# Kernel optimization log

Measured on AMD Instinct MI355X. Metric: run time of the kernel, lower is better.

Reference implementation:

```python
import jax, jax.numpy as jnp
import numpy as np

# dims: T tokens, E experts, D model dim, F ffn dim, C per-expert capacity, K top-k routing
T, E, D, F, C, K = 4096, 8, 1024, 4096, 1536, 2


def setup_inputs() -> dict:
    key = jax.random.key(0)
    k_x, k_lg, k_w1, k_w2 = jax.random.split(key, 4)
    x = jax.random.normal(k_x, (T, D), jnp.float32)
    # external router: top-K of logits per token, softmax weights over kept logits
    logits = jax.random.normal(k_lg, (T, E), jnp.float32)
    topv, topi = jax.lax.top_k(logits, K)                      # (T,K)
    rows = jnp.arange(T)[:, None]
    route_mask = jnp.zeros((T, E), bool).at[rows, topi].set(True)
    route_weight = jnp.zeros((T, E), jnp.float32).at[rows, topi].set(
        jax.nn.softmax(topv, axis=-1))
    # stacked homogeneous expert MLP params (E leading axis, as in _stack_group)
    W1 = jax.random.normal(k_w1, (E, D, F), jnp.float32) / np.sqrt(D)
    b1 = jnp.zeros((E, F), jnp.float32)
    W2 = jax.random.normal(k_w2, (E, F, D), jnp.float32) / np.sqrt(F)
    b2 = jnp.zeros((E, D), jnp.float32)
    return dict(x=x, route_mask=route_mask, route_weight=route_weight,
                W1=W1, b1=b1, W2=W2, b2=b2)


def reference(x, route_mask, route_weight, W1, b1, W2, b2):
    """MoE with per-expert capacity: top-C tokens per expert by route weight,
    gather -> vmapped expert MLP -> weighted scatter-combine.
    Math identical to the one-hot slot einsums ('ect,t...->ec...' dispatch and
    'ecf,ect,te->tf' combine) of the original, expressed as gather/scatter.
    """
    Tn, En = route_mask.shape
    w_te = jnp.where(route_mask, route_weight, 0.0)            # (T,E)
    # per-expert scores; unrouted tokens get -inf so they can never be selected
    w_et = jnp.where(route_mask.T, w_te.T, -jnp.inf)           # (E,T)
    vals, idx = jax.lax.top_k(w_et, C)                         # (E,C) token ids per slot
    valid = jnp.isfinite(vals)                                  # slot actually filled
    # dispatch: gather token features into (E,C,D); empty slots are zero rows
    xe = x[idx] * valid[..., None]
    # grouped expert MLP (vmap over E via batched einsum)
    h = jax.nn.relu(jnp.einsum('ecd,edf->ecf', xe, W1) + b1[:, None, :])
    out = jnp.einsum('ecf,efd->ecd', h, W2) + b2[:, None, :]    # (E,C,D)
    # combine: y[t] = sum over slots assigned to t of w_te[t,e] * out[e,c]
    gain = jnp.where(valid, jnp.take_along_axis(w_te.T, idx, axis=1), 0.0)  # (E,C)
    y = jnp.zeros((Tn, out.shape[-1]), out.dtype)
    y = y.at[idx.reshape(-1)].add((out * gain[..., None]).reshape(-1, out.shape[-1]))
    return y
```

## Files before the change

kernel.cpp:

```cpp
#include <hip/hip_runtime.h>
#include <hip/hip_bf16.h>
#include <stdint.h>

#define T_TOK 4096
#define NE    8
#define DM    1024
#define FF    4096
#define CAP   1536

typedef __attribute__((ext_vector_type(8))) __bf16 bf16x8;
typedef __attribute__((ext_vector_type(4))) float  f32x4;

__device__ __forceinline__ void gload_lds16(const void* gptr, void* lptr) {
  __builtin_amdgcn_global_load_lds(
      (__attribute__((address_space(1))) void*)(uintptr_t)gptr,
      (__attribute__((address_space(3))) void*)(uintptr_t)lptr,
      16, 0, 0);
}


__global__ void conv_x_kernel(const float4* __restrict__ src, ushort4* __restrict__ dst, int n4) {
  int i = blockIdx.x * blockDim.x + threadIdx.x;
  if (i >= n4) return;
  float4 v = src[i];
  ushort4 o;
  o.x = __builtin_bit_cast(unsigned short, __float2bfloat16(v.x));
  o.y = __builtin_bit_cast(unsigned short, __float2bfloat16(v.y));
  o.z = __builtin_bit_cast(unsigned short, __float2bfloat16(v.z));
  o.w = __builtin_bit_cast(unsigned short, __float2bfloat16(v.w));
  dst[i] = o;
}

__global__ __launch_bounds__(256)
void tconv_kernel(const float* __restrict__ src, __hip_bfloat16* __restrict__ dst,
                  int R, int C) {
  __shared__ float tile[64][65];
  const int b  = blockIdx.z;
  const int r0 = blockIdx.y * 64;
  const int c0 = blockIdx.x * 64;
  const float* s = src + (size_t)b * R * C;
  __hip_bfloat16* d = dst + (size_t)b * R * C;
  const int tid = threadIdx.x;
  const int tx = tid & 63, ty = tid >> 6;
#pragma unroll
  for (int rr = ty; rr < 64; rr += 4)
    tile[rr][tx] = s[(size_t)(r0 + rr) * C + c0 + tx];
  __syncthreads();
  const int lg = tid & 15;
  const int cg = tid >> 4;
#pragma unroll
  for (int w = 0; w < 4; ++w) {
    const int cc = w * 16 + cg;
    const int r4 = lg * 4;
    ushort4 o;
    o.x = __builtin_bit_cast(unsigned short, __float2bfloat16(tile[r4 + 0][cc]));
    o.y = __builtin_bit_cast(unsigned short, __float2bfloat16(tile[r4 + 1][cc]));
    o.z = __builtin_bit_cast(unsigned short, __float2bfloat16(tile[r4 + 2][cc]));
    o.w = __builtin_bit_cast(unsigned short, __float2bfloat16(tile[r4 + 3][cc]));
    *(ushort4*)&d[(size_t)(c0 + cc) * R + r0 + r4] = o;
  }
}

__global__ void router_kernel(const float* __restrict__ rw, int* __restrict__ counts,
                              int* __restrict__ tok_ids, float* __restrict__ gains) {
  int t = blockIdx.x * blockDim.x + threadIdx.x;
  if (t >= T_TOK) return;
#pragma unroll
  for (int e = 0; e < NE; ++e) {
    float w = rw[t * NE + e];
    if (w > 0.f) {
      int pos = atomicAdd(&counts[e], 1);
      if (pos < CAP) {
        tok_ids[e * CAP + pos] = t;
        gains[e * CAP + pos]   = w;
      }
    }
  }
}

__global__ void pad_kernel(const int* __restrict__ counts, int* __restrict__ tok_ids,
                           float* __restrict__ gains) {
  int i = blockIdx.x * blockDim.x + threadIdx.x;
  if (i >= NE * CAP) return;
  int e = i / CAP, pos = i % CAP;
  int ne = min(counts[e], CAP);
  if (pos >= ne) { tok_ids[i] = 0; gains[i] = 0.f; }
}


template <int PASS>
__global__ __launch_bounds__(256, 2)
void moe_gemm(const __hip_bfloat16* __restrict__ Asrc,
              const __hip_bfloat16* __restrict__ Bsrc,
              const float* __restrict__ bias,
              const int* __restrict__ counts,
              const int* __restrict__ tok_ids,
              const float* __restrict__ gains,
              __hip_bfloat16* __restrict__ Hout,
              float* __restrict__ y)
{
  constexpr int K  = (PASS == 1) ? DM : FF;
  constexpr int NP = (PASS == 1) ? FF : DM;
  constexpr int MT = CAP / 128;
  constexpr int NT = NP / 128;
  constexpr int KT = K / 64;

  const int bid = blockIdx.x;
  const int e   = bid / (MT * NT);
  const int rem = bid % (MT * NT);
  const int mt  = rem / NT;
  const int nt  = rem % NT;

  const int Ne = min(counts[e], CAP);
  const int m0 = mt * 128;
  if (m0 >= Ne) return;
  const int n0 = nt * 128;

  __shared__ alignas(16) __hip_bfloat16 As[128 * 64];
  __shared__ alignas(16) __hip_bfloat16 Bs[128 * 64];

  const int tid  = threadIdx.x;
  const int lane = tid & 63;
  const int wid  = tid >> 6;
  const int wm   = wid >> 1;
  const int wn   = wid & 1;

  const int srow8 = (tid >> 3) & 7;
  const int cs    = ((tid & 7) ^ srow8) * 8;

  const __hip_bfloat16 *aP[4], *bP[4];
#pragma unroll
  for (int i = 0; i < 4; ++i) {
    const int row = i * 32 + (tid >> 3);
    if (PASS == 1) {
      const int tok = tok_ids[e * CAP + m0 + row];
      aP[i] = Asrc + (size_t)tok * DM + cs;
    } else {
      aP[i] = Asrc + ((size_t)e * CAP + m0 + row) * FF + cs;
    }
    bP[i] = Bsrc + ((size_t)e * NP + n0 + row) * K + cs;
  }

  const char* AsB = (const char*)As;
  const char* BsB = (const char*)Bs;
  const int fr = lane & 15;
  const int fq = lane >> 4;
  const int kb0 = ((fq + 0) ^ (fr & 7)) << 4;
  const int kb1 = ((fq + 4) ^ (fr & 7)) << 4;

  f32x4 acc[4][4] = {};

  for (int kt = 0; kt < KT; ++kt) {
#pragma unroll
    for (int i = 0; i < 4; ++i)
      gload_lds16(aP[i] + kt * 64, (char*)As + i * 4096 + tid * 16);
#pragma unroll
    for (int i = 0; i < 4; ++i)
      gload_lds16(bP[i] + kt * 64, (char*)Bs + i * 4096 + tid * 16);
    __syncthreads();

#pragma unroll
    for (int s = 0; s < 2; ++s) {
      const int kb = s ? kb1 : kb0;
      bf16x8 af[4], bfr[4];
#pragma unroll
      for (int i = 0; i < 4; ++i)
        af[i] = *(const bf16x8*)(AsB + (wm * 64 + i * 16 + fr) * 128 + kb);
#pragma unroll
      for (int j = 0; j < 4; ++j)
        bfr[j] = *(const bf16x8*)(BsB + (wn * 64 + j * 16 + fr) * 128 + kb);
#pragma unroll
      for (int i = 0; i < 4; ++i)
#pragma unroll
        for (int j = 0; j < 4; ++j)
          acc[i][j] = __builtin_amdgcn_mfma_f32_16x16x32_bf16(af[i], bfr[j], acc[i][j], 0, 0, 0);
    }
    __syncthreads();
  }

  const int colb = n0 + wn * 64 + fr;
  if (PASS == 1) {
#pragma unroll
    for (int j = 0; j < 4; ++j) {
      const float bv = bias[(size_t)e * NP + colb + j * 16];
#pragma unroll
      for (int i = 0; i < 4; ++i)
#pragma unroll
        for (int rr = 0; rr < 4; ++rr) {
          const int row = m0 + wm * 64 + i * 16 + fq * 4 + rr;
          float v = acc[i][j][rr] + bv;
          v = v > 0.f ? v : 0.f;
          Hout[((size_t)e * CAP + row) * FF + colb + j * 16] = __float2bfloat16(v);
        }
    }
  } else {
    float bv[4];
#pragma unroll
    for (int j = 0; j < 4; ++j) bv[j] = bias[(size_t)e * NP + colb + j * 16];
#pragma unroll
    for (int i = 0; i < 4; ++i)
#pragma unroll
      for (int rr = 0; rr < 4; ++rr) {
        const int row  = m0 + wm * 64 + i * 16 + fq * 4 + rr;
        const int slot = e * CAP + row;
        const float g  = gains[slot];
        if (g != 0.f) {
          const int tok = tok_ids[slot];
          float* yrow = y + (size_t)tok * DM + colb;
#pragma unroll
          for (int j = 0; j < 4; ++j)
            atomicAdd(yrow + j * 16, (acc[i][j][rr] + bv[j]) * g);
        }
      }
  }
}


extern "C" void kernel_launch(void* const* d_in, const int* in_sizes, int n_in,
                              void* d_out, int out_size, void* d_ws, size_t ws_size,
                              hipStream_t stream) {
  const float* x  = (const float*)d_in[0];
  const float* rw = (const float*)d_in[2];
  const float* W1 = (const float*)d_in[3];
  const float* b1 = (const float*)d_in[4];
  const float* W2 = (const float*)d_in[5];
  const float* b2 = (const float*)d_in[6];
  float* y = (float*)d_out;

  char* ws = (char*)d_ws;
  size_t off = 0;
  auto alloc = [&](size_t bytes) {
    void* p = ws + off;
    off = (off + bytes + 255) & ~(size_t)255;
    return p;
  };
  __hip_bfloat16* xb  = (__hip_bfloat16*)alloc((size_t)T_TOK * DM * 2);
  __hip_bfloat16* w1t = (__hip_bfloat16*)alloc((size_t)NE * DM * FF * 2);
  __hip_bfloat16* w2t = (__hip_bfloat16*)alloc((size_t)NE * FF * DM * 2);
  __hip_bfloat16* Hb  = (__hip_bfloat16*)alloc((size_t)NE * CAP * FF * 2);
  int*   counts  = (int*)alloc(NE * sizeof(int));
  int*   tok_ids = (int*)alloc((size_t)NE * CAP * sizeof(int));
  float* gains   = (float*)alloc((size_t)NE * CAP * sizeof(float));
  (void)ws_size; (void)in_sizes; (void)n_in; (void)out_size;

  hipMemsetAsync(y, 0, (size_t)T_TOK * DM * sizeof(float), stream);
  hipMemsetAsync(counts, 0, NE * sizeof(int), stream);

  conv_x_kernel<<<(T_TOK * DM / 4 + 255) / 256, 256, 0, stream>>>(
      (const float4*)x, (ushort4*)xb, T_TOK * DM / 4);
  tconv_kernel<<<dim3(FF / 64, DM / 64, NE), 256, 0, stream>>>(W1, w1t, DM, FF);
  tconv_kernel<<<dim3(DM / 64, FF / 64, NE), 256, 0, stream>>>(W2, w2t, FF, DM);
  router_kernel<<<(T_TOK + 255) / 256, 256, 0, stream>>>(rw, counts, tok_ids, gains);
  pad_kernel<<<(NE * CAP + 255) / 256, 256, 0, stream>>>(counts, tok_ids, gains);

  moe_gemm<1><<<NE * (CAP / 128) * (FF / 128), 256, 0, stream>>>(
      xb, w1t, b1, counts, tok_ids, gains, Hb, nullptr);
  moe_gemm<2><<<NE * (CAP / 128) * (DM / 128), 256, 0, stream>>>(
      Hb, w2t, b2, counts, tok_ids, gains, nullptr, y);
}
```

Measured before the change: 323.7 us.

## Double-buffer LDS tiles in MoE GEMM with async global-to-LDS prefetch

```diff
diff --git a/kernel.cpp b/kernel.cpp
--- a/kernel.cpp
+++ b/kernel.cpp
@@ -116,8 +116,7 @@
   if (m0 >= Ne) return;
   const int n0 = nt * 128;
 
-  __shared__ alignas(16) __hip_bfloat16 As[128 * 64];
-  __shared__ alignas(16) __hip_bfloat16 Bs[128 * 64];
+  __shared__ alignas(16) char LDSb[65536];
 
   const int tid  = threadIdx.x;
   const int lane = tid & 63;
@@ -141,8 +140,6 @@
     bP[i] = Bsrc + ((size_t)e * NP + n0 + row) * K + cs;
   }
 
-  const char* AsB = (const char*)As;
-  const char* BsB = (const char*)Bs;
   const int fr = lane & 15;
   const int fq = lane >> 4;
   const int kb0 = ((fq + 0) ^ (fr & 7)) << 4;
@@ -150,33 +147,50 @@
 
   f32x4 acc[4][4] = {};
 
-  for (int kt = 0; kt < KT; ++kt) {
-#pragma unroll
-    for (int i = 0; i < 4; ++i)
-      gload_lds16(aP[i] + kt * 64, (char*)As + i * 4096 + tid * 16);
-#pragma unroll
-    for (int i = 0; i < 4; ++i)
-      gload_lds16(bP[i] + kt * 64, (char*)Bs + i * 4096 + tid * 16);
-    __syncthreads();
-
-#pragma unroll
-    for (int s = 0; s < 2; ++s) {
-      const int kb = s ? kb1 : kb0;
-      bf16x8 af[4], bfr[4];
-#pragma unroll
-      for (int i = 0; i < 4; ++i)
-        af[i] = *(const bf16x8*)(AsB + (wm * 64 + i * 16 + fr) * 128 + kb);
-#pragma unroll
-      for (int j = 0; j < 4; ++j)
-        bfr[j] = *(const bf16x8*)(BsB + (wn * 64 + j * 16 + fr) * 128 + kb);
-#pragma unroll
-      for (int i = 0; i < 4; ++i)
-#pragma unroll
-        for (int j = 0; j < 4; ++j)
-          acc[i][j] = __builtin_amdgcn_mfma_f32_16x16x32_bf16(af[i], bfr[j], acc[i][j], 0, 0, 0);
-    }
-    __syncthreads();
-  }
+#define STAGE(d, kt) do {                                                         \
+    _Pragma("unroll") for (int i = 0; i < 4; ++i)                                 \
+      gload_lds16(aP[i] + (kt) * 64, LDSb + (d) * 16384 + i * 4096 + tid * 16);   \
+    _Pragma("unroll") for (int i = 0; i < 4; ++i)                                 \
+      gload_lds16(bP[i] + (kt) * 64, LDSb + 32768 + (d) * 16384 + i * 4096 + tid * 16); \
+  } while (0)
+
+#define COMPUTE(d) do {                                                           \
+    const char* Ab = LDSb + (d) * 16384;                                          \
+    const char* Bb = LDSb + 32768 + (d) * 16384;                                  \
+    _Pragma("unroll") for (int s = 0; s < 2; ++s) {                               \
+      const int kbv = s ? kb1 : kb0;                                              \
+      bf16x8 af[4], bfr[4];                                                       \
+      _Pragma("unroll") for (int i = 0; i < 4; ++i)                               \
+        af[i] = *(const bf16x8*)(Ab + (wm * 64 + i * 16 + fr) * 128 + kbv);       \
+      _Pragma("unroll") for (int j = 0; j < 4; ++j)                               \
+        bfr[j] = *(const bf16x8*)(Bb + (wn * 64 + j * 16 + fr) * 128 + kbv);      \
+      _Pragma("unroll") for (int i = 0; i < 4; ++i)                               \
+        _Pragma("unroll") for (int j = 0; j < 4; ++j)                             \
+          acc[i][j] = __builtin_amdgcn_mfma_f32_16x16x32_bf16(                    \
+              af[i], bfr[j], acc[i][j], 0, 0, 0);                                 \
+    }                                                                             \
+  } while (0)
+
+  STAGE(0, 0);
+  int cur = 0;
+#pragma unroll 1
+  for (int kt = 0; kt < KT - 1; ++kt) {
+    STAGE(cur ^ 1, kt + 1);
+    asm volatile("s_waitcnt vmcnt(8)" ::: "memory");
+    __builtin_amdgcn_s_barrier();
+    __builtin_amdgcn_sched_barrier(0);
+    COMPUTE(cur);
+    __builtin_amdgcn_sched_barrier(0);
+    __builtin_amdgcn_s_barrier();
+    cur ^= 1;
+  }
+  asm volatile("s_waitcnt vmcnt(0)" ::: "memory");
+  __builtin_amdgcn_s_barrier();
+  __builtin_amdgcn_sched_barrier(0);
+  COMPUTE(cur);
+
+#undef STAGE
+#undef COMPUTE
 
   const int colb = n0 + wn * 64 + fr;
   if (PASS == 1) {
```

After: 336.1 us. +3.8%, slower.

## Load MFMA fragments directly from global memory instead of staging through LDS

Applied to the files above, without the earlier changes.

```diff
diff --git a/kernel.cpp b/kernel.cpp
--- a/kernel.cpp
+++ b/kernel.cpp
@@ -10,13 +10,6 @@
 
 typedef __attribute__((ext_vector_type(8))) __bf16 bf16x8;
 typedef __attribute__((ext_vector_type(4))) float  f32x4;
-
-__device__ __forceinline__ void gload_lds16(const void* gptr, void* lptr) {
-  __builtin_amdgcn_global_load_lds(
-      (__attribute__((address_space(1))) void*)(uintptr_t)gptr,
-      (__attribute__((address_space(3))) void*)(uintptr_t)lptr,
-      16, 0, 0);
-}
 
 
 __global__ void conv_x_kernel(const float4* __restrict__ src, ushort4* __restrict__ dst, int n4) {
@@ -89,21 +82,21 @@
 
 
 template <int PASS>
-__global__ __launch_bounds__(256, 2)
-void moe_gemm(const __hip_bfloat16* __restrict__ Asrc,
-              const __hip_bfloat16* __restrict__ Bsrc,
-              const float* __restrict__ bias,
-              const int* __restrict__ counts,
-              const int* __restrict__ tok_ids,
-              const float* __restrict__ gains,
-              __hip_bfloat16* __restrict__ Hout,
-              float* __restrict__ y)
+__global__ __launch_bounds__(256, 4)
+void moe_gemm_direct(const __hip_bfloat16* __restrict__ Asrc,
+                     const __hip_bfloat16* __restrict__ Bsrc,
+                     const float* __restrict__ bias,
+                     const int* __restrict__ counts,
+                     const int* __restrict__ tok_ids,
+                     const float* __restrict__ gains,
+                     __hip_bfloat16* __restrict__ Hout,
+                     float* __restrict__ y)
 {
   constexpr int K  = (PASS == 1) ? DM : FF;
   constexpr int NP = (PASS == 1) ? FF : DM;
   constexpr int MT = CAP / 128;
   constexpr int NT = NP / 128;
-  constexpr int KT = K / 64;
+  constexpr int KT = K / 32;
 
   const int bid = blockIdx.x;
   const int e   = bid / (MT * NT);
@@ -116,66 +109,47 @@
   if (m0 >= Ne) return;
   const int n0 = nt * 128;
 
-  __shared__ alignas(16) __hip_bfloat16 As[128 * 64];
-  __shared__ alignas(16) __hip_bfloat16 Bs[128 * 64];
-
   const int tid  = threadIdx.x;
   const int lane = tid & 63;
   const int wid  = tid >> 6;
   const int wm   = wid >> 1;
   const int wn   = wid & 1;
-
-  const int srow8 = (tid >> 3) & 7;
-  const int cs    = ((tid & 7) ^ srow8) * 8;
-
-  const __hip_bfloat16 *aP[4], *bP[4];
+  const int fr   = lane & 15;
+  const int fq   = lane >> 4;
+
+  const char* Ab = (const char*)Asrc;
+  const char* Bb = (const char*)(Bsrc + (size_t)e * NP * K);
+  uint32_t voA[4], voB[4];
 #pragma unroll
   for (int i = 0; i < 4; ++i) {
-    const int row = i * 32 + (tid >> 3);
+    const int r = m0 + wm * 64 + i * 16 + fr;
     if (PASS == 1) {
-      const int tok = tok_ids[e * CAP + m0 + row];
-      aP[i] = Asrc + (size_t)tok * DM + cs;
+      const int tok = tok_ids[e * CAP + r];
+      voA[i] = (uint32_t)tok * (DM * 2) + fq * 16;
     } else {
-      aP[i] = Asrc + ((size_t)e * CAP + m0 + row) * FF + cs;
+      voA[i] = (uint32_t)r * (FF * 2) + fq * 16;
     }
-    bP[i] = Bsrc + ((size_t)e * NP + n0 + row) * K + cs;
-  }
-
-  const char* AsB = (const char*)As;
-  const char* BsB = (const char*)Bs;
-  const int fr = lane & 15;
-  const int fq = lane >> 4;
-  const int kb0 = ((fq + 0) ^ (fr & 7)) << 4;
-  const int kb1 = ((fq + 4) ^ (fr & 7)) << 4;
+    voB[i] = (uint32_t)(n0 + wn * 64 + i * 16 + fr) * (K * 2) + fq * 16;
+  }
+  if (PASS == 2) Ab = (const char*)(Asrc + (size_t)e * CAP * FF);
 
   f32x4 acc[4][4] = {};
 
+#pragma unroll 4
   for (int kt = 0; kt < KT; ++kt) {
+    const uint32_t kb = (uint32_t)kt * 64;
+    bf16x8 af[4], bfr[4];
 #pragma unroll
     for (int i = 0; i < 4; ++i)
-      gload_lds16(aP[i] + kt * 64, (char*)As + i * 4096 + tid * 16);
+      af[i] = *(const bf16x8*)(Ab + voA[i] + kb);
+#pragma unroll
+    for (int j = 0; j < 4; ++j)
+      bfr[j] = *(const bf16x8*)(Bb + voB[j] + kb);
 #pragma unroll
     for (int i = 0; i < 4; ++i)
-      gload_lds16(bP[i] + kt * 64, (char*)Bs + i * 4096 + tid * 16);
-    __syncthreads();
-
-#pragma unroll
-    for (int s = 0; s < 2; ++s) {
-      const int kb = s ? kb1 : kb0;
-      bf16x8 af[4], bfr[4];
-#pragma unroll
-      for (int i = 0; i < 4; ++i)
-        af[i] = *(const bf16x8*)(AsB + (wm * 64 + i * 16 + fr) * 128 + kb);
 #pragma unroll
       for (int j = 0; j < 4; ++j)
-        bfr[j] = *(const bf16x8*)(BsB + (wn * 64 + j * 16 + fr) * 128 + kb);
-#pragma unroll
-      for (int i = 0; i < 4; ++i)
-#pragma unroll
-        for (int j = 0; j < 4; ++j)
-          acc[i][j] = __builtin_amdgcn_mfma_f32_16x16x32_bf16(af[i], bfr[j], acc[i][j], 0, 0, 0);
-    }
-    __syncthreads();
+        acc[i][j] = __builtin_amdgcn_mfma_f32_16x16x32_bf16(af[i], bfr[j], acc[i][j], 0, 0, 0);
   }
 
   const int colb = n0 + wn * 64 + fr;
@@ -253,8 +227,8 @@
   router_kernel<<<(T_TOK + 255) / 256, 256, 0, stream>>>(rw, counts, tok_ids, gains);
   pad_kernel<<<(NE * CAP + 255) / 256, 256, 0, stream>>>(counts, tok_ids, gains);
 
-  moe_gemm<1><<<NE * (CAP / 128) * (FF / 128), 256, 0, stream>>>(
+  moe_gemm_direct<1><<<NE * (CAP / 128) * (FF / 128), 256, 0, stream>>>(
       xb, w1t, b1, counts, tok_ids, gains, Hb, nullptr);
-  moe_gemm<2><<<NE * (CAP / 128) * (DM / 128), 256, 0, stream>>>(
+  moe_gemm_direct<2><<<NE * (CAP / 128) * (DM / 128), 256, 0, stream>>>(
       Hb, w2t, b2, counts, tok_ids, gains, nullptr, y);
 }
```

Result: slower. 823.6 us (+154.4%).

## Split-K the second expert GEMM and replace pad kernel with memset

Applied to the files above, without the earlier changes.

```diff
diff --git a/kernel.cpp b/kernel.cpp
--- a/kernel.cpp
+++ b/kernel.cpp
@@ -78,18 +78,9 @@
   }
 }
 
-__global__ void pad_kernel(const int* __restrict__ counts, int* __restrict__ tok_ids,
-                           float* __restrict__ gains) {
-  int i = blockIdx.x * blockDim.x + threadIdx.x;
-  if (i >= NE * CAP) return;
-  int e = i / CAP, pos = i % CAP;
-  int ne = min(counts[e], CAP);
-  if (pos >= ne) { tok_ids[i] = 0; gains[i] = 0.f; }
-}
-
-
-template <int PASS>
-__global__ __launch_bounds__(256, 2)
+
+template <int PASS, int SK>
+__global__ __launch_bounds__(256, 4)
 void moe_gemm(const __hip_bfloat16* __restrict__ Asrc,
               const __hip_bfloat16* __restrict__ Bsrc,
               const float* __restrict__ bias,
@@ -103,18 +94,23 @@
   constexpr int NP = (PASS == 1) ? FF : DM;
   constexpr int MT = CAP / 128;
   constexpr int NT = NP / 128;
-  constexpr int KT = K / 64;
-
-  const int bid = blockIdx.x;
-  const int e   = bid / (MT * NT);
-  const int rem = bid % (MT * NT);
-  const int mt  = rem / NT;
-  const int nt  = rem % NT;
+  constexpr int KP = K / SK;
+  constexpr int KT = KP / 64;
+
+  const int bid   = blockIdx.x;
+  const int per_e = MT * NT * SK;
+  const int e     = bid / per_e;
+  int r           = bid % per_e;
+  const int mt    = r / (NT * SK);
+  r               = r % (NT * SK);
+  const int nt    = r / SK;
+  const int sp    = r % SK;
 
   const int Ne = min(counts[e], CAP);
   const int m0 = mt * 128;
   if (m0 >= Ne) return;
   const int n0 = nt * 128;
+  const int k0 = sp * KP;
 
   __shared__ alignas(16) __hip_bfloat16 As[128 * 64];
   __shared__ alignas(16) __hip_bfloat16 Bs[128 * 64];
@@ -134,11 +130,11 @@
     const int row = i * 32 + (tid >> 3);
     if (PASS == 1) {
       const int tok = tok_ids[e * CAP + m0 + row];
-      aP[i] = Asrc + (size_t)tok * DM + cs;
+      aP[i] = Asrc + (size_t)tok * DM + k0 + cs;
     } else {
-      aP[i] = Asrc + ((size_t)e * CAP + m0 + row) * FF + cs;
-    }
-    bP[i] = Bsrc + ((size_t)e * NP + n0 + row) * K + cs;
+      aP[i] = Asrc + ((size_t)e * CAP + m0 + row) * FF + k0 + cs;
+    }
+    bP[i] = Bsrc + ((size_t)e * NP + n0 + row) * K + k0 + cs;
   }
 
   const char* AsB = (const char*)As;
@@ -196,7 +192,8 @@
   } else {
     float bv[4];
 #pragma unroll
-    for (int j = 0; j < 4; ++j) bv[j] = bias[(size_t)e * NP + colb + j * 16];
+    for (int j = 0; j < 4; ++j)
+      bv[j] = (sp == 0) ? bias[(size_t)e * NP + colb + j * 16] : 0.f;
 #pragma unroll
     for (int i = 0; i < 4; ++i)
 #pragma unroll
@@ -244,17 +241,17 @@
   (void)ws_size; (void)in_sizes; (void)n_in; (void)out_size;
 
   hipMemsetAsync(y, 0, (size_t)T_TOK * DM * sizeof(float), stream);
-  hipMemsetAsync(counts, 0, NE * sizeof(int), stream);
+  const size_t ctl_bytes = (size_t)((char*)(gains + NE * CAP) - (char*)counts);
+  hipMemsetAsync(counts, 0, ctl_bytes, stream);
 
   conv_x_kernel<<<(T_TOK * DM / 4 + 255) / 256, 256, 0, stream>>>(
       (const float4*)x, (ushort4*)xb, T_TOK * DM / 4);
   tconv_kernel<<<dim3(FF / 64, DM / 64, NE), 256, 0, stream>>>(W1, w1t, DM, FF);
   tconv_kernel<<<dim3(DM / 64, FF / 64, NE), 256, 0, stream>>>(W2, w2t, FF, DM);
   router_kernel<<<(T_TOK + 255) / 256, 256, 0, stream>>>(rw, counts, tok_ids, gains);
-  pad_kernel<<<(NE * CAP + 255) / 256, 256, 0, stream>>>(counts, tok_ids, gains);
-
-  moe_gemm<1><<<NE * (CAP / 128) * (FF / 128), 256, 0, stream>>>(
+
+  moe_gemm<1, 1><<<NE * (CAP / 128) * (FF / 128), 256, 0, stream>>>(
       xb, w1t, b1, counts, tok_ids, gains, Hb, nullptr);
-  moe_gemm<2><<<NE * (CAP / 128) * (DM / 128), 256, 0, stream>>>(
+  moe_gemm<2, 2><<<NE * (CAP / 128) * (DM / 128) * 2, 256, 0, stream>>>(
       Hb, w2t, b2, counts, tok_ids, gains, nullptr, y);
 }
```

Result: slower. 331.5 us (+2.4%).
